# Kernel optimization log

Measured on AMD Instinct MI355X. Metric: run time of the kernel, lower is better.

The kernel has to match this reference:

```python
import jax, jax.numpy as jnp
import numpy as np

MODEL_DIM = 1024
NUM_HEADS = 16
HEAD_DIM = MODEL_DIM // NUM_HEADS  # 64
MAX_SEQ = 1024
MAX_REL = 8


def setup_inputs() -> dict:
    key = jax.random.key(0)
    ks = jax.random.split(key, 5)
    B, S = 4, 1024
    x = jax.random.normal(ks[0], (B, S, MODEL_DIM), jnp.float32)
    W_in = jax.random.normal(ks[1], (MODEL_DIM, MODEL_DIM), jnp.float32) * 0.02
    W_out = jax.random.normal(ks[2], (MODEL_DIM, MODEL_DIM), jnp.float32) * 0.02
    # learned synthesized attention scores [1, H, max_seq, max_seq]
    attn_scores = jax.random.normal(ks[3], (1, NUM_HEADS, MAX_SEQ, MAX_SEQ), jnp.float32) * 0.05
    # relative-position VALUE embedding table [2*max_rel+1, head_dim]
    rel_values = jax.random.normal(ks[4], (2 * MAX_REL + 1, HEAD_DIM), jnp.float32) * 0.02
    return {"x": x, "W_in": W_in, "W_out": W_out,
            "attn_scores": attn_scores, "rel_values": rel_values}


def reference(x, W_in, W_out, attn_scores, rel_values):
    B, S, D = x.shape
    H, hd = NUM_HEADS, HEAD_DIM
    # in-projection (no bias), split heads: [B, H, S, hd]
    value = (x @ W_in.T).reshape(B, S, H, hd).transpose(0, 2, 1, 3)
    # learned (random-synthesizer) scores, sliced to seq len, broadcast over batch
    scores = attn_scores[:, :, :S, :S]              # [1, H, S, S]
    probs = jax.nn.softmax(scores, axis=-1)          # [1, H, S, S]
    probs = jnp.broadcast_to(probs, (B, H, S, S))
    # attention output: probs @ V
    out = jnp.einsum('bhsj,bhjd->bhsd', probs, value)  # [B, H, S, hd]
    # relative-position value contribution
    r = jnp.arange(S)
    dist = r[None, :] - r[:, None]                   # [S, S]
    idx = jnp.clip(dist, -MAX_REL, MAX_REL) + MAX_REL
    rel_emb = rel_values[idx]                        # [S, S, hd]
    out = out + jnp.einsum('bhsj,sjd->bhsd', probs, rel_emb)
    # join heads and out-project
    out = out.transpose(0, 2, 1, 3).reshape(B, S, H * hd)
    return out @ W_out.T                             # [B, S, D]
```

## Files before the change

kernel.cpp:

```cpp
#include <hip/hip_runtime.h>

typedef unsigned short ushort_t;
typedef __attribute__((ext_vector_type(4))) short short4_t;
typedef __attribute__((ext_vector_type(8))) short short8;
typedef __attribute__((ext_vector_type(4))) float floatx4;
typedef __attribute__((ext_vector_type(8))) __bf16 bf16x8;

__device__ __forceinline__ ushort_t f2b(float f) {
  union { float f; unsigned int i; } t; t.f = f;
  unsigned int u = t.i;
  return (ushort_t)((u + 0x7fffu + ((u >> 16) & 1u)) >> 16);
}

__device__ __forceinline__ floatx4 mfma16(short8 a, short8 b, floatx4 c) {
  return __builtin_amdgcn_mfma_f32_16x16x32_bf16(
      __builtin_bit_cast(bf16x8, a), __builtin_bit_cast(bf16x8, b), c, 0, 0, 0);
}

__device__ __forceinline__ void gload16(const void* g, void* l) {
  __builtin_amdgcn_global_load_lds(
      (const __attribute__((address_space(1))) void*)g,
      (__attribute__((address_space(3))) void*)l, 16, 0, 0);
}

__global__ __launch_bounds__(256) void k_sm_f2b(
    const float* __restrict__ S, const float* __restrict__ relv,
    ushort_t* __restrict__ P, float* __restrict__ R,
    const float* __restrict__ x, const float* __restrict__ Wi,
    const float* __restrict__ Wo, ushort_t* __restrict__ xb,
    ushort_t* __restrict__ Wib, ushort_t* __restrict__ Wob)
{
  __shared__ float mid[4][16];

  if (blockIdx.x < 3072) {
    const float* in; ushort_t* out; int i;
    if (blockIdx.x < 2048)      { in = x;  out = xb;  i = (blockIdx.x * 256 + threadIdx.x) * 8; }
    else if (blockIdx.x < 2560) { in = Wi; out = Wib; i = ((blockIdx.x - 2048) * 256 + threadIdx.x) * 8; }
    else                        { in = Wo; out = Wob; i = ((blockIdx.x - 2560) * 256 + threadIdx.x) * 8; }
    float4 a = *reinterpret_cast<const float4*>(in + i);
    float4 b = *reinterpret_cast<const float4*>(in + i + 4);
    short8 o;
    o[0] = (short)f2b(a.x); o[1] = (short)f2b(a.y);
    o[2] = (short)f2b(a.z); o[3] = (short)f2b(a.w);
    o[4] = (short)f2b(b.x); o[5] = (short)f2b(b.y);
    o[6] = (short)f2b(b.z); o[7] = (short)f2b(b.w);
    *reinterpret_cast<short8*>(out + i) = o;
    return;
  }

  const int wave = threadIdx.x >> 6, lane = threadIdx.x & 63;
  const int row = (blockIdx.x - 3072) * 4 + wave;
  const int s = row & 1023;
  const float* src = S + (size_t)row * 1024;

  float v[4][4];
#pragma unroll
  for (int c = 0; c < 4; ++c) {
    float4 raw = *reinterpret_cast<const float4*>(src + c * 256 + lane * 4);
    v[c][0] = raw.x; v[c][1] = raw.y; v[c][2] = raw.z; v[c][3] = raw.w;
  }
  float m = -1e30f;
#pragma unroll
  for (int c = 0; c < 4; ++c)
#pragma unroll
    for (int e = 0; e < 4; ++e) m = fmaxf(m, v[c][e]);
#pragma unroll
  for (int d = 32; d; d >>= 1) m = fmaxf(m, __shfl_xor(m, d));

  float p[4][4];
  float tot = 0.f, sA = 0.f, sB = 0.f;
#pragma unroll
  for (int c = 0; c < 4; ++c) {
#pragma unroll
    for (int e = 0; e < 4; ++e) {
      int j = c * 256 + lane * 4 + e;
      float pe = __expf(v[c][e] - m);
      p[c][e] = pe;
      tot += pe;
      sA += (j <= s - 8) ? pe : 0.f;
      sB += (j >= s + 8) ? pe : 0.f;
    }
  }
#pragma unroll
  for (int d = 32; d; d >>= 1) {
    tot += __shfl_xor(tot, d);
    sA  += __shfl_xor(sA, d);
    sB  += __shfl_xor(sB, d);
  }
  const float inv = 1.0f / tot;

  if (lane < 16) mid[wave][lane] = 0.f;
  __syncthreads();
#pragma unroll
  for (int c = 0; c < 4; ++c) {
#pragma unroll
    for (int e = 0; e < 4; ++e) {
      int j = c * 256 + lane * 4 + e;
      int tt = j - (s - 7);
      if (tt >= 0 && tt < 15) mid[wave][tt] = p[c][e];
    }
  }
  __syncthreads();

  float acc = sA * relv[lane] + sB * relv[16 * 64 + lane];
#pragma unroll
  for (int tt = 0; tt < 15; ++tt)
    acc += mid[wave][tt] * relv[(1 + tt) * 64 + lane];
  R[(size_t)row * 64 + lane] = acc * inv;

#pragma unroll
  for (int c = 0; c < 4; ++c) {
    short4_t o;
#pragma unroll
    for (int e = 0; e < 4; ++e) o[e] = (short)f2b(p[c][e] * inv);
    *reinterpret_cast<short4_t*>(P + (size_t)row * 1024 + c * 256 + lane * 4) = o;
  }
}

#define STG(kt, buf)                                                        \
  {                                                                         \
    const int k0 = (kt) << 6;                                               \
    _Pragma("unroll")                                                       \
    for (int cc = 0; cc < 2; ++cc) {                                        \
      int c = threadIdx.x + (cc << 9);                                      \
      int r = c >> 3, cb = c & 7;                                           \
      int sc = k0 + ((cb ^ (r & 7)) << 3);                                  \
      gload16(A0 + (size_t)r * 1024 + sc, (char*)sA + (buf) * 16384 + c * 16); \
      gload16(B0 + (size_t)r * 1024 + sc, (char*)sB + (buf) * 16384 + c * 16); \
    }                                                                       \
  }

#define KSTEP_COMPUTE(bA, bB)                                               \
  _Pragma("unroll")                                                         \
  for (int kk = 0; kk < 2; ++kk) {                                          \
    const int cs = (kk << 2) + lk;                                          \
    short8 af[4], bf[2];                                                    \
    _Pragma("unroll")                                                       \
    for (int i = 0; i < 4; ++i) {                                           \
      int ra = (wm << 6) + (i << 4) + l15;                                  \
      af[i] = *reinterpret_cast<const short8*>(                             \
          (bA) + ra * 128 + ((cs ^ (ra & 7)) << 4));                        \
    }                                                                       \
    _Pragma("unroll")                                                       \
    for (int j = 0; j < 2; ++j) {                                           \
      int rb = (wn << 5) + (j << 4) + l15;                                  \
      bf[j] = *reinterpret_cast<const short8*>(                             \
          (bB) + rb * 128 + ((cs ^ (rb & 7)) << 4));                        \
    }                                                                       \
    __builtin_amdgcn_s_setprio(1);                                          \
    _Pragma("unroll")                                                       \
    for (int i = 0; i < 4; ++i)                                             \
      _Pragma("unroll")                                                     \
      for (int j = 0; j < 2; ++j)                                           \
        acc[i][j] = mfma16(af[i], bf[j], acc[i][j]);                        \
    __builtin_amdgcn_s_setprio(0);                                          \
  }

__device__ __forceinline__ void gemm128_loop4(
    const ushort_t* __restrict__ A0, const ushort_t* __restrict__ B0,
    ushort_t* sA, ushort_t* sB, floatx4 (&acc)[4][2])
{
  const int lane = threadIdx.x & 63, wave = threadIdx.x >> 6;
  const int wm = wave & 1, wn = wave >> 1;
  const int l15 = lane & 15, lk = lane >> 4;

  STG(0, 0);
  STG(1, 1);
  for (int kt = 0; kt < 16; ++kt) {
    if (kt < 14) {
      STG(kt + 2, (kt + 2) & 3);
      asm volatile("s_waitcnt vmcnt(8)" ::: "memory");
    } else if (kt == 14) {
      asm volatile("s_waitcnt vmcnt(4)" ::: "memory");
    } else {
      asm volatile("s_waitcnt vmcnt(0)" ::: "memory");
    }
    __builtin_amdgcn_s_barrier();
    const char* bA = (const char*)sA + (kt & 3) * 16384;
    const char* bB = (const char*)sB + (kt & 3) * 16384;
    KSTEP_COMPUTE(bA, bB);
  }
}

__device__ __forceinline__ int xcd_swz(int bid) {
  return ((bid & 7) << 5) | (bid >> 3);
}

__global__ __launch_bounds__(512) void k_gemm_xw(
    const ushort_t* __restrict__ W, const ushort_t* __restrict__ X,
    ushort_t* __restrict__ Yt)
{
  __shared__ ushort_t sA[4 * 128 * 64];
  __shared__ ushort_t sB[4 * 128 * 64];
  const int lg = xcd_swz(blockIdx.x);
  const int m0 = (lg & 7) << 7, n0 = (lg >> 3) << 7;
  const ushort_t* A0 = W + (size_t)m0 * 1024;
  const ushort_t* B0 = X + (size_t)n0 * 1024;
  floatx4 acc[4][2] = {};
  gemm128_loop4(A0, B0, sA, sB, acc);

  const int lane = threadIdx.x & 63, wave = threadIdx.x >> 6;
  const int wm = wave & 1, wn = wave >> 1;
  const int l15 = lane & 15, lk = lane >> 4;
#pragma unroll
  for (int i = 0; i < 4; ++i)
#pragma unroll
    for (int j = 0; j < 2; ++j)
#pragma unroll
      for (int rr = 0; rr < 4; ++rr) {
        int wrow = m0 + (wm << 6) + (i << 4) + (lk << 2) + rr;
        int col  = n0 + (wn << 5) + (j << 4) + l15;
        int h = wrow >> 6, d = wrow & 63;
        int b = col >> 10, s = col & 1023;
        Yt[(((size_t)((h << 2) + b) << 6) + d) * 1024 + s] = f2b(acc[i][j][rr]);
      }
}

__global__ __launch_bounds__(512) void k_head_pv(
    const ushort_t* __restrict__ P, const ushort_t* __restrict__ Yt,
    const float* __restrict__ R, ushort_t* __restrict__ O)
{
  __shared__ ushort_t sA[4 * 128 * 64];
  __shared__ ushort_t sB[4 * 128 * 64];
  const int lg = xcd_swz(blockIdx.x);
  const int h = lg >> 4, rem = lg & 15;
  const int m0 = (rem >> 1) << 7, n0 = (rem & 1) << 7;
  const ushort_t* A0 = P + ((size_t)h << 20) + (size_t)m0 * 1024;
  const ushort_t* B0 = Yt + ((size_t)h << 18) + (size_t)n0 * 1024;
  floatx4 acc[4][2] = {};
  gemm128_loop4(A0, B0, sA, sB, acc);

  const int lane = threadIdx.x & 63, wave = threadIdx.x >> 6;
  const int wm = wave & 1, wn = wave >> 1;
  const int l15 = lane & 15, lk = lane >> 4;
#pragma unroll
  for (int i = 0; i < 4; ++i)
#pragma unroll
    for (int j = 0; j < 2; ++j)
#pragma unroll
      for (int rr = 0; rr < 4; ++rr) {
        int sr = m0 + (wm << 6) + (i << 4) + (lk << 2) + rr;
        int c  = n0 + (wn << 5) + (j << 4) + l15;
        int b = c >> 6, d = c & 63;
        float val = acc[i][j][rr] + R[(((size_t)h << 10) + sr) * 64 + d];
        O[((size_t)b << 20) + ((size_t)sr << 10) + (h << 6) + d] = f2b(val);
      }
}

__global__ __launch_bounds__(512) void k_gemm_out(
    const ushort_t* __restrict__ A, const ushort_t* __restrict__ B,
    float* __restrict__ C)
{
  __shared__ ushort_t sA[4 * 128 * 64];
  __shared__ ushort_t sB[4 * 128 * 64];
  const int lg = xcd_swz(blockIdx.x);
  const int m0 = (lg >> 3) << 7, n0 = (lg & 7) << 7;
  const ushort_t* A0 = A + (size_t)m0 * 1024;
  const ushort_t* B0 = B + (size_t)n0 * 1024;
  floatx4 acc[4][2] = {};
  gemm128_loop4(A0, B0, sA, sB, acc);

  const int lane = threadIdx.x & 63, wave = threadIdx.x >> 6;
  const int wm = wave & 1, wn = wave >> 1;
  const int l15 = lane & 15, lk = lane >> 4;
#pragma unroll
  for (int i = 0; i < 4; ++i)
#pragma unroll
    for (int j = 0; j < 2; ++j)
#pragma unroll
      for (int rr = 0; rr < 4; ++rr) {
        int rowg = m0 + (wm << 6) + (i << 4) + (lk << 2) + rr;
        int colg = n0 + (wn << 5) + (j << 4) + l15;
        C[(size_t)rowg * 1024 + colg] = acc[i][j][rr];
      }
}

extern "C" void kernel_launch(void* const* d_in, const int* in_sizes, int n_in,
                              void* d_out, int out_size, void* d_ws, size_t ws_size,
                              hipStream_t stream)
{
  const float* x     = (const float*)d_in[0];
  const float* W_in  = (const float*)d_in[1];
  const float* W_out = (const float*)d_in[2];
  const float* attn  = (const float*)d_in[3];
  const float* relv  = (const float*)d_in[4];
  float* out = (float*)d_out;

  char* ws = (char*)d_ws;
  ushort_t* xb  = (ushort_t*)(ws);
  ushort_t* Wib = (ushort_t*)(ws + (8u << 20));
  ushort_t* Wob = (ushort_t*)(ws + (10u << 20));
  ushort_t* P   = (ushort_t*)(ws + (12u << 20));
  float*    R   = (float*)   (ws + (44u << 20));
  ushort_t* Yt  = (ushort_t*)(ws + (48u << 20));
  ushort_t* O   = (ushort_t*)(ws + (56u << 20));

  k_sm_f2b<<<7168, 256, 0, stream>>>(attn, relv, P, R, x, W_in, W_out, xb, Wib, Wob);
  k_gemm_xw<<<256, 512, 0, stream>>>(Wib, xb, Yt);
  k_head_pv<<<256, 512, 0, stream>>>(P, Yt, R, O);
  k_gemm_out<<<256, 512, 0, stream>>>(O, Wob, out);
}
```

Measured before the change: 64.97 us.

## Fuse x fp32-to-bf16 conversion into in-projection GEMM B-operand loading

Drops the separate pass that converts x to bf16 in the prologue kernel. The in-projection GEMM now reads fp32 x straight into registers, converts it, and writes swizzled bf16 into LDS. The A operand still uses direct global-to-LDS loads. Pipelining drops from a 4-stage async buffer to double-buffering with register staging, and the 32 MB fp32 read is repeated across the 8 M-tiles that share each x tile. This removes one write and one read of the bf16 copy of x but adds conversion work and register pressure inside the GEMM.

```diff
diff --git a/kernel.cpp b/kernel.cpp
--- a/kernel.cpp
+++ b/kernel.cpp
@@ -11,6 +11,10 @@
   unsigned int u = t.i;
   return (ushort_t)((u + 0x7fffu + ((u >> 16) & 1u)) >> 16);
 }
+__device__ __forceinline__ ushort_t cvtb(float f) {
+  __bf16 h = (__bf16)f;
+  return __builtin_bit_cast(unsigned short, h);
+}
 
 __device__ __forceinline__ floatx4 mfma16(short8 a, short8 b, floatx4 c) {
   return __builtin_amdgcn_mfma_f32_16x16x32_bf16(
@@ -23,20 +27,18 @@
       (__attribute__((address_space(3))) void*)l, 16, 0, 0);
 }
 
-__global__ __launch_bounds__(256) void k_sm_f2b(
+__global__ __launch_bounds__(256) void k_sm_f2bw(
     const float* __restrict__ S, const float* __restrict__ relv,
     ushort_t* __restrict__ P, float* __restrict__ R,
-    const float* __restrict__ x, const float* __restrict__ Wi,
-    const float* __restrict__ Wo, ushort_t* __restrict__ xb,
+    const float* __restrict__ Wi, const float* __restrict__ Wo,
     ushort_t* __restrict__ Wib, ushort_t* __restrict__ Wob)
 {
   __shared__ float mid[4][16];
 
-  if (blockIdx.x < 3072) {
+  if (blockIdx.x < 1024) {
     const float* in; ushort_t* out; int i;
-    if (blockIdx.x < 2048)      { in = x;  out = xb;  i = (blockIdx.x * 256 + threadIdx.x) * 8; }
-    else if (blockIdx.x < 2560) { in = Wi; out = Wib; i = ((blockIdx.x - 2048) * 256 + threadIdx.x) * 8; }
-    else                        { in = Wo; out = Wob; i = ((blockIdx.x - 2560) * 256 + threadIdx.x) * 8; }
+    if (blockIdx.x < 512) { in = Wi; out = Wib; i = (blockIdx.x * 256 + threadIdx.x) * 8; }
+    else                  { in = Wo; out = Wob; i = ((blockIdx.x - 512) * 256 + threadIdx.x) * 8; }
     float4 a = *reinterpret_cast<const float4*>(in + i);
     float4 b = *reinterpret_cast<const float4*>(in + i + 4);
     short8 o;
@@ -49,7 +51,7 @@
   }
 
   const int wave = threadIdx.x >> 6, lane = threadIdx.x & 63;
-  const int row = (blockIdx.x - 3072) * 4 + wave;
+  const int row = (blockIdx.x - 1024) * 4 + wave;
   const int s = row & 1023;
   const float* src = S + (size_t)row * 1024;
 
@@ -187,21 +189,76 @@
 }
 
 __global__ __launch_bounds__(512) void k_gemm_xw(
-    const ushort_t* __restrict__ W, const ushort_t* __restrict__ X,
+    const ushort_t* __restrict__ W, const float* __restrict__ Xf,
     ushort_t* __restrict__ Yt)
 {
-  __shared__ ushort_t sA[4 * 128 * 64];
-  __shared__ ushort_t sB[4 * 128 * 64];
+  __shared__ ushort_t sA[2 * 128 * 64];
+  __shared__ ushort_t sB[2 * 128 * 64];
   const int lg = xcd_swz(blockIdx.x);
   const int m0 = (lg & 7) << 7, n0 = (lg >> 3) << 7;
   const ushort_t* A0 = W + (size_t)m0 * 1024;
-  const ushort_t* B0 = X + (size_t)n0 * 1024;
-  floatx4 acc[4][2] = {};
-  gemm128_loop4(A0, B0, sA, sB, acc);
+  const float*    Bf = Xf + (size_t)n0 * 1024;
 
   const int lane = threadIdx.x & 63, wave = threadIdx.x >> 6;
   const int wm = wave & 1, wn = wave >> 1;
   const int l15 = lane & 15, lk = lane >> 4;
+  floatx4 acc[4][2] = {};
+  float4 breg[4];
+
+#define STGA(kt, buf)                                                       \
+  {                                                                         \
+    const int k0 = (kt) << 6;                                               \
+    _Pragma("unroll")                                                       \
+    for (int cc = 0; cc < 2; ++cc) {                                        \
+      int c = threadIdx.x + (cc << 9);                                      \
+      int r = c >> 3, cb = c & 7;                                           \
+      int sc = k0 + ((cb ^ (r & 7)) << 3);                                  \
+      gload16(A0 + (size_t)r * 1024 + sc, (char*)sA + (buf) * 16384 + c * 16); \
+    }                                                                       \
+  }
+#define LOADB(kt)                                                           \
+  {                                                                         \
+    const int k0 = (kt) << 6;                                               \
+    _Pragma("unroll")                                                       \
+    for (int cc = 0; cc < 2; ++cc) {                                        \
+      int c = threadIdx.x + (cc << 9);                                      \
+      int r = c >> 3, cb = c & 7;                                           \
+      int sc = k0 + ((cb ^ (r & 7)) << 3);                                  \
+      const float* srcp = Bf + (size_t)r * 1024 + sc;                       \
+      breg[cc * 2]     = *reinterpret_cast<const float4*>(srcp);            \
+      breg[cc * 2 + 1] = *reinterpret_cast<const float4*>(srcp + 4);        \
+    }                                                                       \
+  }
+#define CVTW(buf)                                                           \
+  {                                                                         \
+    _Pragma("unroll")                                                       \
+    for (int cc = 0; cc < 2; ++cc) {                                        \
+      int c = threadIdx.x + (cc << 9);                                      \
+      float4 va = breg[cc * 2], vb = breg[cc * 2 + 1];                      \
+      short8 o;                                                             \
+      o[0] = (short)cvtb(va.x); o[1] = (short)cvtb(va.y);                   \
+      o[2] = (short)cvtb(va.z); o[3] = (short)cvtb(va.w);                   \
+      o[4] = (short)cvtb(vb.x); o[5] = (short)cvtb(vb.y);                   \
+      o[6] = (short)cvtb(vb.z); o[7] = (short)cvtb(vb.w);                   \
+      *reinterpret_cast<short8*>((char*)sB + (buf) * 16384 + c * 16) = o;   \
+    }                                                                       \
+  }
+
+  STGA(0, 0);
+  LOADB(0);
+  CVTW(0);
+  for (int kt = 0; kt < 16; ++kt) {
+    __syncthreads();
+    if (kt < 15) { STGA(kt + 1, (kt + 1) & 1); LOADB(kt + 1); }
+    const char* bA = (const char*)sA + (kt & 1) * 16384;
+    const char* bB = (const char*)sB + (kt & 1) * 16384;
+    KSTEP_COMPUTE(bA, bB);
+    if (kt < 15) CVTW((kt + 1) & 1);
+  }
+#undef STGA
+#undef LOADB
+#undef CVTW
+
 #pragma unroll
   for (int i = 0; i < 4; ++i)
 #pragma unroll
@@ -287,7 +344,6 @@
   float* out = (float*)d_out;
 
   char* ws = (char*)d_ws;
-  ushort_t* xb  = (ushort_t*)(ws);
   ushort_t* Wib = (ushort_t*)(ws + (8u << 20));
   ushort_t* Wob = (ushort_t*)(ws + (10u << 20));
   ushort_t* P   = (ushort_t*)(ws + (12u << 20));
@@ -295,8 +351,8 @@
   ushort_t* Yt  = (ushort_t*)(ws + (48u << 20));
   ushort_t* O   = (ushort_t*)(ws + (56u << 20));
 
-  k_sm_f2b<<<7168, 256, 0, stream>>>(attn, relv, P, R, x, W_in, W_out, xb, Wib, Wob);
-  k_gemm_xw<<<256, 512, 0, stream>>>(Wib, xb, Yt);
+  k_sm_f2bw<<<5120, 256, 0, stream>>>(attn, relv, P, R, W_in, W_out, Wib, Wob);
+  k_gemm_xw<<<256, 512, 0, stream>>>(Wib, x, Yt);
   k_head_pv<<<256, 512, 0, stream>>>(P, Yt, R, O);
   k_gemm_out<<<256, 512, 0, stream>>>(O, Wob, out);
 }
```

Measured after the change: 70.03 us. +7.8%, slower.

## Overlap part of softmax preprocessing with the X·W GEMM via extra producer waves

Applied to the files above, without the earlier changes.

Moves the softmax and relative-value reduction for half of the score rows (rows 8192 onward) out of the preprocessing kernel and into four extra waves appended to each block of the input-projection GEMM. Those waves compute the row softmax, write bf16 probabilities and the relative-position contribution concurrently with the MFMA GEMM waves. The preprocessing grid shrinks to match. The aim is to hide memory-bound softmax work behind the compute-bound GEMM, at the cost of higher register and occupancy pressure in a 768-thread block. There is also barrier-count coupling: the softmax waves call s_barrier 16 times while the GEMM waves return early.

```diff
diff --git a/kernel.cpp b/kernel.cpp
--- a/kernel.cpp
+++ b/kernel.cpp
@@ -186,34 +186,129 @@
   return ((bid & 7) << 5) | (bid >> 3);
 }
 
-__global__ __launch_bounds__(512) void k_gemm_xw(
+__global__ __launch_bounds__(768) void k_gemm_xw_sm(
     const ushort_t* __restrict__ W, const ushort_t* __restrict__ X,
-    ushort_t* __restrict__ Yt)
+    ushort_t* __restrict__ Yt,
+    const float* __restrict__ S, const float* __restrict__ relv,
+    ushort_t* __restrict__ P, float* __restrict__ R)
 {
   __shared__ ushort_t sA[4 * 128 * 64];
   __shared__ ushort_t sB[4 * 128 * 64];
-  const int lg = xcd_swz(blockIdx.x);
-  const int m0 = (lg & 7) << 7, n0 = (lg >> 3) << 7;
-  const ushort_t* A0 = W + (size_t)m0 * 1024;
-  const ushort_t* B0 = X + (size_t)n0 * 1024;
-  floatx4 acc[4][2] = {};
-  gemm128_loop4(A0, B0, sA, sB, acc);
-
-  const int lane = threadIdx.x & 63, wave = threadIdx.x >> 6;
-  const int wm = wave & 1, wn = wave >> 1;
-  const int l15 = lane & 15, lk = lane >> 4;
-#pragma unroll
-  for (int i = 0; i < 4; ++i)
-#pragma unroll
-    for (int j = 0; j < 2; ++j)
-#pragma unroll
-      for (int rr = 0; rr < 4; ++rr) {
-        int wrow = m0 + (wm << 6) + (i << 4) + (lk << 2) + rr;
-        int col  = n0 + (wn << 5) + (j << 4) + l15;
-        int h = wrow >> 6, d = wrow & 63;
-        int b = col >> 10, s = col & 1023;
-        Yt[(((size_t)((h << 2) + b) << 6) + d) * 1024 + s] = f2b(acc[i][j][rr]);
-      }
+  const int t = threadIdx.x;
+
+  if (t < 512) {
+    const int lg = xcd_swz(blockIdx.x);
+    const int m0 = (lg & 7) << 7, n0 = (lg >> 3) << 7;
+    const ushort_t* A0 = W + (size_t)m0 * 1024;
+    const ushort_t* B0 = X + (size_t)n0 * 1024;
+    floatx4 acc[4][2] = {};
+    gemm128_loop4(A0, B0, sA, sB, acc);
+
+    const int lane = t & 63, wave = t >> 6;
+    const int wm = wave & 1, wn = wave >> 1;
+    const int l15 = lane & 15, lk = lane >> 4;
+#pragma unroll
+    for (int i = 0; i < 4; ++i)
+#pragma unroll
+      for (int j = 0; j < 2; ++j)
+#pragma unroll
+        for (int rr = 0; rr < 4; ++rr) {
+          int wrow = m0 + (wm << 6) + (i << 4) + (lk << 2) + rr;
+          int col  = n0 + (wn << 5) + (j << 4) + l15;
+          int h = wrow >> 6, d = wrow & 63;
+          int b = col >> 10, s = col & 1023;
+          Yt[(((size_t)((h << 2) + b) << 6) + d) * 1024 + s] = f2b(acc[i][j][rr]);
+        }
+    return;
+  }
+
+  const int lane = t & 63;
+  const int rowbase = 8192 + blockIdx.x * 32 + ((t >> 6) - 8) * 8;
+  float4 a0, a1, b0, b1;
+
+  for (int sl = 0; sl < 16; ++sl) {
+    __builtin_amdgcn_s_barrier();
+    const int row = rowbase + (sl >> 1);
+    const float* src = S + ((size_t)row << 10) + (lane << 3);
+    if ((sl & 1) == 0) {
+      a0 = *reinterpret_cast<const float4*>(src);
+      a1 = *reinterpret_cast<const float4*>(src + 4);
+      b0 = *reinterpret_cast<const float4*>(src + 512);
+      b1 = *reinterpret_cast<const float4*>(src + 516);
+    } else {
+      const int s = row & 1023;
+      float p0[8] = {a0.x, a0.y, a0.z, a0.w, a1.x, a1.y, a1.z, a1.w};
+      float p1[8] = {b0.x, b0.y, b0.z, b0.w, b1.x, b1.y, b1.z, b1.w};
+      float m = -3e38f;
+#pragma unroll
+      for (int e = 0; e < 8; ++e) m = fmaxf(m, fmaxf(p0[e], p1[e]));
+#pragma unroll
+      for (int dd = 32; dd; dd >>= 1) m = fmaxf(m, __shfl_xor(m, dd));
+      float tot = 0.f, sa = 0.f, sb = 0.f;
+#pragma unroll
+      for (int e = 0; e < 8; ++e) {
+        int c0 = (lane << 3) + e, c1 = 512 + (lane << 3) + e;
+        float e0 = __expf(p0[e] - m), e1 = __expf(p1[e] - m);
+        p0[e] = e0; p1[e] = e1;
+        tot += e0 + e1;
+        sa += ((c0 <= s - 8) ? e0 : 0.f) + ((c1 <= s - 8) ? e1 : 0.f);
+        sb += ((c0 >= s + 8) ? e0 : 0.f) + ((c1 >= s + 8) ? e1 : 0.f);
+      }
+#pragma unroll
+      for (int dd = 32; dd; dd >>= 1) {
+        tot += __shfl_xor(tot, dd);
+        sa  += __shfl_xor(sa, dd);
+        sb  += __shfl_xor(sb, dd);
+      }
+      const float inv = 1.0f / tot;
+      float accR = sa * relv[lane] + sb * relv[16 * 64 + lane];
+      const int lo = (s - 7 < 0) ? 0 : s - 7;
+      const int hi = (s + 7 > 1023) ? 1023 : s + 7;
+      {
+        int ch = (hi < 511) ? hi : 511;
+        if (lo <= ch) {
+          int g0 = lo >> 3, g1 = ch >> 3;
+          for (int gi = 0; gi < 3; ++gi) {
+            int g = g0 + gi;
+            if (g > g1) break;
+#pragma unroll
+            for (int e = 0; e < 8; ++e) {
+              float val = __shfl(p0[e], g);
+              int col = (g << 3) + e;
+              if (col >= lo && col <= hi)
+                accR += val * relv[(8 + col - s) * 64 + lane];
+            }
+          }
+        }
+      }
+      {
+        int cl = (lo > 512) ? lo : 512;
+        if (cl <= hi) {
+          int g0 = (cl - 512) >> 3, g1 = (hi - 512) >> 3;
+          for (int gi = 0; gi < 3; ++gi) {
+            int g = g0 + gi;
+            if (g > g1) break;
+#pragma unroll
+            for (int e = 0; e < 8; ++e) {
+              float val = __shfl(p1[e], g);
+              int col = 512 + (g << 3) + e;
+              if (col >= lo && col <= hi)
+                accR += val * relv[(8 + col - s) * 64 + lane];
+            }
+          }
+        }
+      }
+      R[((size_t)row << 6) + lane] = accR * inv;
+      short8 o0, o1;
+#pragma unroll
+      for (int e = 0; e < 8; ++e) {
+        o0[e] = (short)f2b(p0[e] * inv);
+        o1[e] = (short)f2b(p1[e] * inv);
+      }
+      *reinterpret_cast<short8*>(P + ((size_t)row << 10) + (lane << 3)) = o0;
+      *reinterpret_cast<short8*>(P + ((size_t)row << 10) + 512 + (lane << 3)) = o1;
+    }
+  }
 }
 
 __global__ __launch_bounds__(512) void k_head_pv(
@@ -295,8 +390,8 @@
   ushort_t* Yt  = (ushort_t*)(ws + (48u << 20));
   ushort_t* O   = (ushort_t*)(ws + (56u << 20));
 
-  k_sm_f2b<<<7168, 256, 0, stream>>>(attn, relv, P, R, x, W_in, W_out, xb, Wib, Wob);
-  k_gemm_xw<<<256, 512, 0, stream>>>(Wib, xb, Yt);
+  k_sm_f2b<<<5120, 256, 0, stream>>>(attn, relv, P, R, x, W_in, W_out, xb, Wib, Wob);
+  k_gemm_xw_sm<<<256, 768, 0, stream>>>(Wib, xb, Yt, attn, relv, P, R);
   k_head_pv<<<256, 512, 0, stream>>>(P, Yt, R, O);
   k_gemm_out<<<256, 512, 0, stream>>>(O, Wob, out);
 }
```

After: 84.42 us. +29.9%, slower.

## Fuse three GEMM launches into one kernel with global atomic barriers

Applied to the files above, without the earlier changes.

Merges the in-projection GEMM, the per-head PV GEMM and the out-projection GEMM into a single 256-block kernel. The phases are separated by a software grid barrier built on atomic counters and spin-waits. This is meant to remove two kernel launch gaps and the tail and ramp idle time between dependent GEMMs. It relies on all 256 blocks being resident at once. The counters live in the last bytes of the output buffer, which the final phase overwrites while slower blocks may still be polling, so correctness is fragile.

```diff
diff --git a/kernel.cpp b/kernel.cpp
--- a/kernel.cpp
+++ b/kernel.cpp
@@ -186,93 +186,93 @@
   return ((bid & 7) << 5) | (bid >> 3);
 }
 
-__global__ __launch_bounds__(512) void k_gemm_xw(
-    const ushort_t* __restrict__ W, const ushort_t* __restrict__ X,
-    ushort_t* __restrict__ Yt)
+__device__ __forceinline__ void gbar(unsigned* flag, unsigned target) {
+  __syncthreads();
+  if (threadIdx.x == 0) {
+    __threadfence();
+    __hip_atomic_fetch_add(flag, 1u, __ATOMIC_RELEASE, __HIP_MEMORY_SCOPE_AGENT);
+    while (__hip_atomic_load(flag, __ATOMIC_RELAXED, __HIP_MEMORY_SCOPE_AGENT) < target)
+      __builtin_amdgcn_s_sleep(8);
+    __threadfence();
+  }
+  __syncthreads();
+}
+
+__global__ __launch_bounds__(512) void k_gemm3(
+    const ushort_t* __restrict__ Wib, const ushort_t* __restrict__ xb,
+    ushort_t* __restrict__ Yt,
+    const ushort_t* __restrict__ P, const float* __restrict__ R,
+    ushort_t* __restrict__ O,
+    const ushort_t* __restrict__ Wob, float* __restrict__ out,
+    unsigned* __restrict__ flags)
 {
   __shared__ ushort_t sA[4 * 128 * 64];
   __shared__ ushort_t sB[4 * 128 * 64];
   const int lg = xcd_swz(blockIdx.x);
-  const int m0 = (lg & 7) << 7, n0 = (lg >> 3) << 7;
-  const ushort_t* A0 = W + (size_t)m0 * 1024;
-  const ushort_t* B0 = X + (size_t)n0 * 1024;
-  floatx4 acc[4][2] = {};
-  gemm128_loop4(A0, B0, sA, sB, acc);
-
   const int lane = threadIdx.x & 63, wave = threadIdx.x >> 6;
   const int wm = wave & 1, wn = wave >> 1;
   const int l15 = lane & 15, lk = lane >> 4;
-#pragma unroll
-  for (int i = 0; i < 4; ++i)
-#pragma unroll
-    for (int j = 0; j < 2; ++j)
-#pragma unroll
-      for (int rr = 0; rr < 4; ++rr) {
-        int wrow = m0 + (wm << 6) + (i << 4) + (lk << 2) + rr;
-        int col  = n0 + (wn << 5) + (j << 4) + l15;
-        int h = wrow >> 6, d = wrow & 63;
-        int b = col >> 10, s = col & 1023;
-        Yt[(((size_t)((h << 2) + b) << 6) + d) * 1024 + s] = f2b(acc[i][j][rr]);
-      }
-}
-
-__global__ __launch_bounds__(512) void k_head_pv(
-    const ushort_t* __restrict__ P, const ushort_t* __restrict__ Yt,
-    const float* __restrict__ R, ushort_t* __restrict__ O)
-{
-  __shared__ ushort_t sA[4 * 128 * 64];
-  __shared__ ushort_t sB[4 * 128 * 64];
-  const int lg = xcd_swz(blockIdx.x);
-  const int h = lg >> 4, rem = lg & 15;
-  const int m0 = (rem >> 1) << 7, n0 = (rem & 1) << 7;
-  const ushort_t* A0 = P + ((size_t)h << 20) + (size_t)m0 * 1024;
-  const ushort_t* B0 = Yt + ((size_t)h << 18) + (size_t)n0 * 1024;
-  floatx4 acc[4][2] = {};
-  gemm128_loop4(A0, B0, sA, sB, acc);
-
-  const int lane = threadIdx.x & 63, wave = threadIdx.x >> 6;
-  const int wm = wave & 1, wn = wave >> 1;
-  const int l15 = lane & 15, lk = lane >> 4;
-#pragma unroll
-  for (int i = 0; i < 4; ++i)
-#pragma unroll
-    for (int j = 0; j < 2; ++j)
-#pragma unroll
-      for (int rr = 0; rr < 4; ++rr) {
-        int sr = m0 + (wm << 6) + (i << 4) + (lk << 2) + rr;
-        int c  = n0 + (wn << 5) + (j << 4) + l15;
-        int b = c >> 6, d = c & 63;
-        float val = acc[i][j][rr] + R[(((size_t)h << 10) + sr) * 64 + d];
-        O[((size_t)b << 20) + ((size_t)sr << 10) + (h << 6) + d] = f2b(val);
-      }
-}
-
-__global__ __launch_bounds__(512) void k_gemm_out(
-    const ushort_t* __restrict__ A, const ushort_t* __restrict__ B,
-    float* __restrict__ C)
-{
-  __shared__ ushort_t sA[4 * 128 * 64];
-  __shared__ ushort_t sB[4 * 128 * 64];
-  const int lg = xcd_swz(blockIdx.x);
-  const int m0 = (lg >> 3) << 7, n0 = (lg & 7) << 7;
-  const ushort_t* A0 = A + (size_t)m0 * 1024;
-  const ushort_t* B0 = B + (size_t)n0 * 1024;
-  floatx4 acc[4][2] = {};
-  gemm128_loop4(A0, B0, sA, sB, acc);
-
-  const int lane = threadIdx.x & 63, wave = threadIdx.x >> 6;
-  const int wm = wave & 1, wn = wave >> 1;
-  const int l15 = lane & 15, lk = lane >> 4;
-#pragma unroll
-  for (int i = 0; i < 4; ++i)
-#pragma unroll
-    for (int j = 0; j < 2; ++j)
-#pragma unroll
-      for (int rr = 0; rr < 4; ++rr) {
-        int rowg = m0 + (wm << 6) + (i << 4) + (lk << 2) + rr;
-        int colg = n0 + (wn << 5) + (j << 4) + l15;
-        C[(size_t)rowg * 1024 + colg] = acc[i][j][rr];
-      }
+
+  {
+    const int m0 = (lg & 7) << 7, n0 = (lg >> 3) << 7;
+    const ushort_t* A0 = Wib + (size_t)m0 * 1024;
+    const ushort_t* B0 = xb + (size_t)n0 * 1024;
+    floatx4 acc[4][2] = {};
+    gemm128_loop4(A0, B0, sA, sB, acc);
+#pragma unroll
+    for (int i = 0; i < 4; ++i)
+#pragma unroll
+      for (int j = 0; j < 2; ++j)
+#pragma unroll
+        for (int rr = 0; rr < 4; ++rr) {
+          int wrow = m0 + (wm << 6) + (i << 4) + (lk << 2) + rr;
+          int col  = n0 + (wn << 5) + (j << 4) + l15;
+          int h = wrow >> 6, d = wrow & 63;
+          int b = col >> 10, s = col & 1023;
+          Yt[(((size_t)((h << 2) + b) << 6) + d) * 1024 + s] = f2b(acc[i][j][rr]);
+        }
+  }
+  gbar(flags + 0, 256u);
+
+  {
+    const int h = lg >> 4, rem = lg & 15;
+    const int m0 = (rem >> 1) << 7, n0 = (rem & 1) << 7;
+    const ushort_t* A0 = P + ((size_t)h << 20) + (size_t)m0 * 1024;
+    const ushort_t* B0 = Yt + ((size_t)h << 18) + (size_t)n0 * 1024;
+    floatx4 acc[4][2] = {};
+    gemm128_loop4(A0, B0, sA, sB, acc);
+#pragma unroll
+    for (int i = 0; i < 4; ++i)
+#pragma unroll
+      for (int j = 0; j < 2; ++j)
+#pragma unroll
+        for (int rr = 0; rr < 4; ++rr) {
+          int sr = m0 + (wm << 6) + (i << 4) + (lk << 2) + rr;
+          int c  = n0 + (wn << 5) + (j << 4) + l15;
+          int b = c >> 6, d = c & 63;
+          float val = acc[i][j][rr] + R[(((size_t)h << 10) + sr) * 64 + d];
+          O[((size_t)b << 20) + ((size_t)sr << 10) + (h << 6) + d] = f2b(val);
+        }
+  }
+  gbar(flags + 1, 256u);
+
+  {
+    const int m0 = (lg >> 3) << 7, n0 = (lg & 7) << 7;
+    const ushort_t* A0 = O + (size_t)m0 * 1024;
+    const ushort_t* B0 = Wob + (size_t)n0 * 1024;
+    floatx4 acc[4][2] = {};
+    gemm128_loop4(A0, B0, sA, sB, acc);
+#pragma unroll
+    for (int i = 0; i < 4; ++i)
+#pragma unroll
+      for (int j = 0; j < 2; ++j)
+#pragma unroll
+        for (int rr = 0; rr < 4; ++rr) {
+          int rowg = m0 + (wm << 6) + (i << 4) + (lk << 2) + rr;
+          int colg = n0 + (wn << 5) + (j << 4) + l15;
+          out[(size_t)rowg * 1024 + colg] = acc[i][j][rr];
+        }
+  }
 }
 
 extern "C" void kernel_launch(void* const* d_in, const int* in_sizes, int n_in,
@@ -295,8 +295,9 @@
   ushort_t* Yt  = (ushort_t*)(ws + (48u << 20));
   ushort_t* O   = (ushort_t*)(ws + (56u << 20));
 
+  unsigned* flags = (unsigned*)((char*)d_out + (size_t)out_size * 4 - 64);
+  hipMemsetAsync(flags, 0, 64, stream);
+
   k_sm_f2b<<<7168, 256, 0, stream>>>(attn, relv, P, R, x, W_in, W_out, xb, Wib, Wob);
-  k_gemm_xw<<<256, 512, 0, stream>>>(Wib, xb, Yt);
-  k_head_pv<<<256, 512, 0, stream>>>(P, Yt, R, O);
-  k_gemm_out<<<256, 512, 0, stream>>>(O, Wob, out);
-}
+  k_gemm3<<<256, 512, 0, stream>>>(Wib, xb, Yt, P, R, O, Wob, out, flags);
+}
```

Measured after the change: 114.2 us. 1.76x slower.
